# Kernel optimization log

Hardware: AMD Instinct MI355X
Metric: run time of the kernel (lower is better)

## Reference

```python
import jax, jax.numpy as jnp
import numpy as np

N_NODES = 50000
N_EDGES = 600000
N_GRAPHS = 512
HID = 128
LAT = 64
L = 4
BN_EPS = 1e-5


def _gelu(x):
    return jax.nn.gelu(x, approximate=False)


def _bn(x, g, b):
    m = jnp.mean(x, axis=0)
    v = jnp.var(x, axis=0)
    return (x - m) * jax.lax.rsqrt(v + BN_EPS) * g + b


def setup_inputs() -> dict:
    key = jax.random.key(0)
    ks = jax.random.split(key, 8)
    x = jax.random.normal(ks[0], (N_NODES, HID), dtype=jnp.float32)
    edge_index = jax.random.randint(ks[1], (2, N_EDGES), 0, N_NODES, dtype=jnp.int64 if jax.config.jax_enable_x64 else jnp.int32)
    batch = jnp.sort(jax.random.randint(ks[2], (N_NODES,), 0, N_GRAPHS))
    scale = 1.0 / np.sqrt(HID)
    return {
        "x": x,
        "edge_index": edge_index,
        "batch": batch,
        "input_bn_g": jnp.ones((HID,), jnp.float32),
        "input_bn_b": jnp.zeros((HID,), jnp.float32),
        "eps": jnp.zeros((L,), jnp.float32),
        "fc1_w": jax.random.normal(ks[3], (L, HID, HID), jnp.float32) * scale,
        "fc1_b": jnp.zeros((L, HID), jnp.float32),
        "bn1_g": jnp.ones((L, HID), jnp.float32),
        "bn1_b": jnp.zeros((L, HID), jnp.float32),
        "fc2_w": jax.random.normal(ks[4], (L, HID, HID), jnp.float32) * scale,
        "fc2_b": jnp.zeros((L, HID), jnp.float32),
        "bn_g": jnp.ones((L, HID), jnp.float32),
        "bn_b": jnp.zeros((L, HID), jnp.float32),
        "att_weight": jax.random.normal(ks[5], (L, HID), jnp.float32),
        "pool_weight": jnp.ones((3,), jnp.float32),
        "fcA_w": jax.random.normal(ks[6], (HID, HID), jnp.float32) * scale,
        "fcA_b": jnp.zeros((HID,), jnp.float32),
        "ln_g": jnp.ones((HID,), jnp.float32),
        "ln_b": jnp.zeros((HID,), jnp.float32),
        "fcB_w": jax.random.normal(ks[7], (HID, LAT), jnp.float32) * scale,
        "fcB_b": jnp.zeros((LAT,), jnp.float32),
    }


def reference(x, edge_index, batch, input_bn_g, input_bn_b, eps, fc1_w, fc1_b,
              bn1_g, bn1_b, fc2_w, fc2_b, bn_g, bn_b, att_weight, pool_weight,
              fcA_w, fcA_b, ln_g, ln_b, fcB_w, fcB_b):
    src, dst = edge_index[0], edge_index[1]
    x = _bn(x, input_bn_g, input_bn_b)  # input BatchNorm (batch stats)
    hidden_states = []
    for l in range(L):
        # GINConv: (1+eps)*x_i + sum_{j->i} x_j, then GatedResidualMLP
        agg = jax.ops.segment_sum(x[src], dst, num_segments=N_NODES)
        h = (1.0 + eps[l]) * x + agg
        h = _gelu(_bn(h @ fc1_w[l] + fc1_b[l], bn1_g[l], bn1_b[l]))
        h = h @ fc2_w[l] + fc2_b[l]
        h = _gelu(_bn(h, bn_g[l], bn_b[l]))
        hidden_states.append(h)
        x = h
    # JumpingKnowledge attention over layers
    x_all = jnp.stack(hidden_states, axis=0)               # [L, N, H]
    scores = jnp.mean(x_all * att_weight[:, None, :], -1)  # [L, N]
    alpha = jax.nn.softmax(scores, axis=0)
    x = jnp.sum(x_all * alpha[..., None], axis=0)          # [N, H]
    # fused add/mean/max pooling by graph id
    pw = jax.nn.softmax(pool_weight)
    sums = jax.ops.segment_sum(x, batch, num_segments=N_GRAPHS)
    cnt = jax.ops.segment_sum(jnp.ones((N_NODES, 1), x.dtype), batch, num_segments=N_GRAPHS)
    mean = sums / jnp.maximum(cnt, 1.0)
    mx = jax.ops.segment_max(x, batch, num_segments=N_GRAPHS)
    mx = jnp.where(cnt > 0, mx, 0.0)
    pooled = sums * pw[0] + mean * pw[1] + mx * pw[2]      # [G, H]
    out = pooled @ fcA_w + fcA_b
    mu = jnp.mean(out, -1, keepdims=True)
    var = jnp.var(out, -1, keepdims=True)
    out = (out - mu) * jax.lax.rsqrt(var + 1e-5) * ln_g + ln_b
    out = _gelu(out) + pooled
    return out @ fcB_w + fcB_b                              # [G, latent]
```

## Files before the change

### kernel.cpp

```cpp
#include <hip/hip_runtime.h>
#include <math.h>

#define N_NODES 50000
#define N_EDGES 600000
#define N_GRAPHS 512
#define HID 128
#define LAT 64
#define NL 4
#define SSTR 16
#define SSET 4096
#define N_TILES 3125
#define TLD 72

typedef __attribute__((ext_vector_type(8))) __bf16 bf16x8;
typedef __attribute__((ext_vector_type(4))) float f32x4;

union Chunk {
    bf16x8 v;
    uint4 u4;
    ushort us[8];
};

__device__ __forceinline__ float gelu_exact(float x) {
    return 0.5f * x * (1.0f + erff(x * 0.70710678118654752f));
}
__device__ __forceinline__ float gelu_fast(float x) {
    float ax = fabsf(x) * 0.70710678118654752f;
    float t = __builtin_amdgcn_rcpf(fmaf(0.3275911f, ax, 1.0f));
    float p = t * (0.254829592f +
              t * (-0.284496736f +
              t * (1.421413741f +
              t * (-1.453152027f + t * 1.061405429f))));
    float e = __expf(-ax * ax);
    float erfv = 1.0f - p * e;
    float erfs = copysignf(erfv, x);
    return 0.5f * x * (1.0f + erfs);
}
__device__ __forceinline__ float bf2f(ushort h) {
    return __uint_as_float(((unsigned int)h) << 16);
}
__device__ __forceinline__ ushort f2bf(float f) {
    unsigned int u = __float_as_uint(f);
    unsigned int r = (u + 0x7FFFu + ((u >> 16) & 1u)) >> 16;
    return (ushort)r;
}
__device__ __forceinline__ void atomicMaxF(float* addr, float v) {
    if (v >= 0.f) atomicMax((int*)addr, __float_as_int(v));
    else atomicMin((unsigned int*)addr, __float_as_uint(v));
}

__device__ __forceinline__ void sub_range(int p, int j, int& s0, int& s1) {
    int r0 = (p * N_NODES) >> 8;
    int r1 = ((p + 1) * N_NODES) >> 8;
    int len = r1 - r0;
    s0 = r0 + ((len * j) >> 3);
    s1 = r0 + ((len * (j + 1)) >> 3);
}

__global__ __launch_bounds__(256) void wt_build(const float* __restrict__ fc1w,
                                                const float* __restrict__ fc2w,
                                                ushort* __restrict__ Wt) {
    int i = blockIdx.x * 256 + threadIdx.x;
    if (i >= 8 * HID * HID) return;
    int g = i >> 14;
    int rem = i & 16383;
    int n = rem >> 7, k = rem & 127;
    const float* W = (g < 4) ? (fc1w + (long)g * HID * HID) : (fc2w + (long)(g - 4) * HID * HID);
    Wt[i] = f2bf(W[k * HID + n]);
}

__global__ __launch_bounds__(256) void col_stats(const float* __restrict__ X,
                                                 float* __restrict__ stats) {
    __shared__ float sh[2048];
    int t = threadIdx.x;
    int tx = t & 31, ty = t >> 5;
    float s[4] = {0, 0, 0, 0}, q[4] = {0, 0, 0, 0};
    const int nTiles = (N_NODES + 63) / 64;
    for (int tile = blockIdx.x; tile < nTiles; tile += gridDim.x) {
        int r0 = tile * 64;
#pragma unroll
        for (int i = 0; i < 8; ++i) {
            int r = r0 + ty + 8 * i;
            int rc = min(r, N_NODES - 1);
            float4 v = *(const float4*)(X + (long)rc * HID + 4 * tx);
            float w = (r < N_NODES) ? 1.f : 0.f;
            float x0 = v.x * w, x1 = v.y * w, x2 = v.z * w, x3 = v.w * w;
            s[0] += x0; s[1] += x1; s[2] += x2; s[3] += x3;
            q[0] += x0 * v.x; q[1] += x1 * v.y; q[2] += x2 * v.z; q[3] += x3 * v.w;
        }
    }
#pragma unroll
    for (int c = 0; c < 4; ++c) {
        sh[ty * HID + 4 * tx + c] = s[c];
        sh[1024 + ty * HID + 4 * tx + c] = q[c];
    }
    __syncthreads();
    if (ty == 0) {
#pragma unroll
        for (int c = 0; c < 4; ++c) {
            float a = 0, b = 0;
#pragma unroll
            for (int j = 0; j < 8; ++j) {
                a += sh[j * HID + 4 * tx + c];
                b += sh[1024 + j * HID + 4 * tx + c];
            }
            atomicAdd(stats + (4 * tx + c) * SSTR, a);
            atomicAdd(stats + (HID + 4 * tx + c) * SSTR, b);
        }
    }
}

__global__ __launch_bounds__(256) void bn_apply_f32(const float* __restrict__ X,
                                                    ushort* __restrict__ Y,
                                                    const float* __restrict__ stats,
                                                    const float* __restrict__ g,
                                                    const float* __restrict__ b) {
    __shared__ float scL[HID], sfL[HID];
    int t = threadIdx.x;
    if (t < HID) {
        const float invN = 1.0f / (float)N_NODES;
        float mean = stats[t * SSTR] * invN;
        float var = stats[(HID + t) * SSTR] * invN - mean * mean;
        float s = g[t] * rsqrtf(var + 1e-5f);
        scL[t] = s;
        sfL[t] = b[t] - mean * s;
    }
    __syncthreads();
    int c4 = (t & 31) * 4;
    float sc[4], sf[4];
#pragma unroll
    for (int j = 0; j < 4; ++j) { sc[j] = scL[c4 + j]; sf[j] = sfL[c4 + j]; }
    int s0, s1;
    sub_range(blockIdx.x & 255, blockIdx.x >> 8, s0, s1);
    int c0 = s0 * 32, c1 = s1 * 32;
    for (int i = c0 + t; i < c1; i += 256) {
        float4 v = ((const float4*)X)[i];
        ushort4 w;
        w.x = f2bf(v.x * sc[0] + sf[0]);
        w.y = f2bf(v.y * sc[1] + sf[1]);
        w.z = f2bf(v.z * sc[2] + sf[2]);
        w.w = f2bf(v.w * sc[3] + sf[3]);
        ((ushort4*)Y)[i] = w;
    }
}

__global__ __launch_bounds__(256) void bn_apply_bf(const ushort* __restrict__ X,
                                                   ushort* __restrict__ Y,
                                                   const float* __restrict__ stats,
                                                   const float* __restrict__ g,
                                                   const float* __restrict__ b) {
    __shared__ float scL[HID], sfL[HID];
    int t = threadIdx.x;
    if (t < HID) {
        const float invN = 1.0f / (float)N_NODES;
        float mean = stats[t * SSTR] * invN;
        float var = stats[(HID + t) * SSTR] * invN - mean * mean;
        float s = g[t] * rsqrtf(var + 1e-5f);
        scL[t] = s;
        sfL[t] = b[t] - mean * s;
    }
    __syncthreads();
    int c8 = (t & 15) * 8;
    float sc[8], sf[8];
#pragma unroll
    for (int j = 0; j < 8; ++j) { sc[j] = scL[c8 + j]; sf[j] = sfL[c8 + j]; }
    int s0, s1;
    sub_range(blockIdx.x & 255, blockIdx.x >> 8, s0, s1);
    int c0 = s0 * 16, c1 = s1 * 16;
    for (int i = c0 + t; i < c1; i += 256) {
        Chunk ch;
        ch.u4 = ((const uint4*)X)[i];
#pragma unroll
        for (int j = 0; j < 8; ++j) {
            float f = bf2f(ch.us[j]) * sc[j] + sf[j];
            ch.us[j] = f2bf(gelu_fast(f));
        }
        ((uint4*)Y)[i] = ch.u4;
    }
}

__global__ __launch_bounds__(256) void csr_count(const int* __restrict__ dst,
                                                 int* __restrict__ counts) {
    int e = blockIdx.x * blockDim.x + threadIdx.x;
    if (e >= N_EDGES) return;
    atomicAdd(counts + dst[e], 1);
}

__global__ __launch_bounds__(256) void scan_pass1(const int* __restrict__ counts,
                                                  int* __restrict__ offs,
                                                  int* __restrict__ bsum) {
    __shared__ int sh[256];
    int t = threadIdx.x;
    int i = blockIdx.x * 256 + t;
    int v = (i < N_NODES) ? counts[i] : 0;
    sh[t] = v;
    __syncthreads();
    for (int off = 1; off < 256; off <<= 1) {
        int a = (t >= off) ? sh[t - off] : 0;
        __syncthreads();
        sh[t] += a;
        __syncthreads();
    }
    if (i < N_NODES) offs[i] = sh[t] - v;
    if (t == 255) bsum[blockIdx.x] = sh[255];
}

__global__ __launch_bounds__(256) void scan_pass2(int* __restrict__ bsum, int nblk) {
    __shared__ int sh[256];
    int t = threadIdx.x;
    int v = (t < nblk) ? bsum[t] : 0;
    sh[t] = v;
    __syncthreads();
    for (int off = 1; off < 256; off <<= 1) {
        int a = (t >= off) ? sh[t - off] : 0;
        __syncthreads();
        sh[t] += a;
        __syncthreads();
    }
    if (t < nblk) bsum[t] = sh[t] - v;
}

__global__ __launch_bounds__(256) void scan_pass3(int* __restrict__ offs,
                                                  const int* __restrict__ bsum,
                                                  int* __restrict__ cursor) {
    int i = blockIdx.x * 256 + threadIdx.x;
    if (i >= N_NODES) return;
    int o = offs[i] + bsum[blockIdx.x];
    offs[i] = o;
    cursor[i] = o;
}

__global__ __launch_bounds__(256) void csr_fill(const int* __restrict__ src,
                                                const int* __restrict__ dst,
                                                int* __restrict__ cursor,
                                                int* __restrict__ csr) {
    int e = blockIdx.x * blockDim.x + threadIdx.x;
    if (e >= N_EDGES) return;
    int pos = atomicAdd(cursor + dst[e], 1);
    csr[pos] = src[e];
}

__global__ __launch_bounds__(256) void gin_gather_bf(const ushort* __restrict__ Xbf,
                                                     ushort* __restrict__ Hp,
                                                     const int* __restrict__ offs,
                                                     const int* __restrict__ counts,
                                                     const int* __restrict__ csr,
                                                     const float* __restrict__ eps, int l) {
    int t = threadIdx.x;
    int tx = t & 31;
    int grp = t >> 5;
    int s0, s1;
    sub_range(blockIdx.x & 255, blockIdx.x >> 8, s0, s1);
    float ev = 1.0f + eps[l];
    for (int node = s0 + grp; node < s1; node += 8) {
        ushort4 sv = *(const ushort4*)(Xbf + (long)node * HID + 4 * tx);
        float a0 = bf2f(sv.x) * ev, a1 = bf2f(sv.y) * ev;
        float a2 = bf2f(sv.z) * ev, a3 = bf2f(sv.w) * ev;
        int o = offs[node];
        int d = counts[node];
        int k = 0;
        for (; k + 8 <= d; k += 8) {
            int si[8];
#pragma unroll
            for (int j = 0; j < 8; ++j) si[j] = csr[o + k + j];
            ushort4 v[8];
#pragma unroll
            for (int j = 0; j < 8; ++j)
                v[j] = *(const ushort4*)(Xbf + (long)si[j] * HID + 4 * tx);
#pragma unroll
            for (int j = 0; j < 8; ++j) {
                a0 += bf2f(v[j].x); a1 += bf2f(v[j].y);
                a2 += bf2f(v[j].z); a3 += bf2f(v[j].w);
            }
        }
        for (; k + 4 <= d; k += 4) {
            int si[4];
#pragma unroll
            for (int j = 0; j < 4; ++j) si[j] = csr[o + k + j];
#pragma unroll
            for (int j = 0; j < 4; ++j) {
                ushort4 v = *(const ushort4*)(Xbf + (long)si[j] * HID + 4 * tx);
                a0 += bf2f(v.x); a1 += bf2f(v.y); a2 += bf2f(v.z); a3 += bf2f(v.w);
            }
        }
        for (; k < d; ++k) {
            int s = csr[o + k];
            ushort4 v = *(const ushort4*)(Xbf + (long)s * HID + 4 * tx);
            a0 += bf2f(v.x); a1 += bf2f(v.y); a2 += bf2f(v.z); a3 += bf2f(v.w);
        }
        ushort4 w;
        w.x = f2bf(a0); w.y = f2bf(a1); w.z = f2bf(a2); w.w = f2bf(a3);
        *(ushort4*)(Hp + (long)node * HID + 4 * tx) = w;
    }
}

__global__ __launch_bounds__(256, 1) void gemm_persist(
    const ushort* __restrict__ Abf, const ushort* __restrict__ Wt,
    const float* __restrict__ bias, ushort* __restrict__ Cbf,
    const float* __restrict__ statsIn, const float* __restrict__ gIn,
    const float* __restrict__ bIn, int applyIn, float* __restrict__ statsOut) {
    __shared__ float scL[HID], sfL[HID];
    __shared__ __align__(16) ushort T[4][16 * TLD];
    __shared__ float shs[8 * 64];
    int t = threadIdx.x;
    if (applyIn && t < HID) {
        const float invN = 1.0f / (float)N_NODES;
        float mean = statsIn[t * SSTR] * invN;
        float var = statsIn[(HID + t) * SSTR] * invN - mean * mean;
        float s = gIn[t] * rsqrtf(var + 1e-5f);
        scL[t] = s;
        sfL[t] = bIn[t] - mean * s;
    }
    __syncthreads();

    int w = t >> 6, lane = t & 63;
    int m = lane & 15, q = lane >> 4;
    int c2 = w & 1, r2 = w >> 1;
    ushort* Tw = T[w];

    const ushort* Wh = Wt + (long)(c2 * 64) * HID;
    bf16x8 Bfrag[4][4];
#pragma unroll
    for (int nt = 0; nt < 4; ++nt)
#pragma unroll
        for (int kc = 0; kc < 4; ++kc)
            Bfrag[nt][kc] = *(const bf16x8*)(Wh + (nt * 16 + m) * HID + kc * 32 + q * 8);

    float bias4[4];
#pragma unroll
    for (int nt = 0; nt < 4; ++nt) bias4[nt] = bias[c2 * 64 + nt * 16 + m];

    float s_col[4], q_col[4];
#pragma unroll
    for (int nt = 0; nt < 4; ++nt) { s_col[nt] = 0.f; q_col[nt] = 0.f; }

    int t0 = (blockIdx.x * N_TILES) >> 8;
    int t1 = ((blockIdx.x + 1) * N_TILES) >> 8;

    int tile = t0 + r2;
    Chunk Ac[4];
    if (tile < t1) {
        const ushort* arow = Abf + (long)(tile * 16 + m) * HID + q * 8;
#pragma unroll
        for (int kc = 0; kc < 4; ++kc) Ac[kc].u4 = *(const uint4*)(arow + kc * 32);
    }
    while (tile < t1) {
        int nxt = tile + 2;
        Chunk An[4];
        if (nxt < t1) {
            const ushort* arow = Abf + (long)(nxt * 16 + m) * HID + q * 8;
#pragma unroll
            for (int kc = 0; kc < 4; ++kc) An[kc].u4 = *(const uint4*)(arow + kc * 32);
        }
        if (applyIn) {
#pragma unroll
            for (int kc = 0; kc < 4; ++kc)
#pragma unroll
                for (int j = 0; j < 8; ++j) {
                    int k = kc * 32 + q * 8 + j;
                    float f = bf2f(Ac[kc].us[j]) * scL[k] + sfL[k];
                    Ac[kc].us[j] = f2bf(gelu_fast(f));
                }
        }
        f32x4 acc[4];
#pragma unroll
        for (int nt = 0; nt < 4; ++nt) acc[nt] = (f32x4){0.f, 0.f, 0.f, 0.f};
#pragma unroll
        for (int kc = 0; kc < 4; ++kc)
#pragma unroll
            for (int nt = 0; nt < 4; ++nt)
                acc[nt] = __builtin_amdgcn_mfma_f32_16x16x32_bf16(Ac[kc].v, Bfrag[nt][kc],
                                                                  acc[nt], 0, 0, 0);
#pragma unroll
        for (int nt = 0; nt < 4; ++nt) {
            int col = nt * 16 + m;
#pragma unroll
            for (int r = 0; r < 4; ++r) {
                float z = acc[nt][r] + bias4[nt];
                Tw[(q * 4 + r) * TLD + col] = f2bf(z);
                s_col[nt] += z;
                q_col[nt] += z * z;
            }
        }
        long cbase = (long)(tile * 16) * HID + c2 * 64;
#pragma unroll
        for (int i = 0; i < 2; ++i) {
            int slot = i * 64 + lane;
            int row = slot >> 3, off = slot & 7;
            uint4 vv = *(const uint4*)(Tw + row * TLD + off * 8);
            *(uint4*)(Cbf + cbase + (long)row * HID + off * 8) = vv;
        }
        tile = nxt;
#pragma unroll
        for (int kc = 0; kc < 4; ++kc) Ac[kc] = An[kc];
    }

#pragma unroll
    for (int nt = 0; nt < 4; ++nt) {
        s_col[nt] += __shfl_xor(s_col[nt], 16);
        s_col[nt] += __shfl_xor(s_col[nt], 32);
        q_col[nt] += __shfl_xor(q_col[nt], 16);
        q_col[nt] += __shfl_xor(q_col[nt], 32);
    }
    if (q == 0) {
#pragma unroll
        for (int nt = 0; nt < 4; ++nt) {
            shs[w * 64 + nt * 16 + m] = s_col[nt];
            shs[256 + w * 64 + nt * 16 + m] = q_col[nt];
        }
    }
    __syncthreads();
    if (t < HID) {
        int half = t >> 6, lc = t & 63;
        float a = shs[half * 64 + lc] + shs[(2 + half) * 64 + lc];
        float b = shs[256 + half * 64 + lc] + shs[256 + (2 + half) * 64 + lc];
        atomicAdd(statsOut + t * SSTR, a);
        atomicAdd(statsOut + (HID + t) * SSTR, b);
    }
}

__global__ __launch_bounds__(256) void pool_init(float* __restrict__ psum,
                                                 float* __restrict__ pmax,
                                                 int* __restrict__ gstart,
                                                 int* __restrict__ gend) {
    int i = blockIdx.x * 256 + threadIdx.x;
    if (i < N_GRAPHS) { gstart[i] = 0; gend[i] = 0; }
    if (i >= N_GRAPHS * HID) return;
    psum[i] = 0.f;
    pmax[i] = -INFINITY;
}

__global__ __launch_bounds__(256) void jk_pool(const ushort* __restrict__ H0,
                                               const ushort* __restrict__ H1,
                                               const ushort* __restrict__ H2,
                                               const ushort* __restrict__ H3,
                                               const float* __restrict__ att,
                                               const int* __restrict__ batch,
                                               float* __restrict__ psum,
                                               float* __restrict__ pmax) {
    int t = threadIdx.x;
    int lane = t & 63, w = t >> 6;
    long wid = (long)blockIdx.x * 4 + w;
    int a0 = (int)((wid * N_NODES) >> 13);
    int a1 = (int)(((wid + 1) * N_NODES) >> 13);
    const ushort* Hs[4] = {H0, H1, H2, H3};
    float2 av[4];
#pragma unroll
    for (int l = 0; l < 4; ++l) av[l] = *(const float2*)(att + l * HID + 2 * lane);

    int curg = -1;
    float sx = 0.f, sy = 0.f, mx = -INFINITY, my = -INFINITY;
    for (int node = a0; node < a1; ++node) {
        int g = batch[node];
        if (g != curg) {
            if (curg >= 0) {
                float* ps = psum + (long)curg * HID + 2 * lane;
                float* pm = pmax + (long)curg * HID + 2 * lane;
                atomicAdd(ps, sx);
                atomicAdd(ps + 1, sy);
                atomicMaxF(pm, mx);
                atomicMaxF(pm + 1, my);
            }
            curg = g;
            sx = 0.f; sy = 0.f; mx = -INFINITY; my = -INFINITY;
        }
        float hx[4], hy[4], scr[4];
#pragma unroll
        for (int l = 0; l < 4; ++l) {
            unsigned int u = *(const unsigned int*)(Hs[l] + (long)node * HID + 2 * lane);
            float vx = bf2f((ushort)(u & 0xFFFF));
            float vy = bf2f((ushort)(u >> 16));
            hx[l] = vx; hy[l] = vy;
            float p = vx * av[l].x + vy * av[l].y;
#pragma unroll
            for (int off = 32; off > 0; off >>= 1) p += __shfl_xor(p, off);
            scr[l] = p * (1.0f / HID);
        }
        float mm = fmaxf(fmaxf(scr[0], scr[1]), fmaxf(scr[2], scr[3]));
        float e[4], se = 0.f;
#pragma unroll
        for (int l = 0; l < 4; ++l) { e[l] = expf(scr[l] - mm); se += e[l]; }
        float inv = 1.0f / se;
        float ox = 0.f, oy = 0.f;
#pragma unroll
        for (int l = 0; l < 4; ++l) {
            float a = e[l] * inv;
            ox += a * hx[l];
            oy += a * hy[l];
        }
        sx += ox; sy += oy;
        mx = fmaxf(mx, ox); my = fmaxf(my, oy);
    }
    if (curg >= 0) {
        float* ps = psum + (long)curg * HID + 2 * lane;
        float* pm = pmax + (long)curg * HID + 2 * lane;
        atomicAdd(ps, sx);
        atomicAdd(ps + 1, sy);
        atomicMaxF(pm, mx);
        atomicMaxF(pm + 1, my);
    }
}

__global__ __launch_bounds__(128) void pool_finalize(const float* __restrict__ psum,
                                                     const float* __restrict__ pmax,
                                                     const int* __restrict__ gstart,
                                                     const int* __restrict__ gend,
                                                     const float* __restrict__ pw,
                                                     float* __restrict__ pooled) {
    int g = blockIdx.x, f = threadIdx.x;
    float w0 = pw[0], w1 = pw[1], w2 = pw[2];
    float m = fmaxf(w0, fmaxf(w1, w2));
    float e0 = expf(w0 - m), e1 = expf(w1 - m), e2 = expf(w2 - m);
    float inv = 1.0f / (e0 + e1 + e2);
    e0 *= inv; e1 *= inv; e2 *= inv;
    int cnt = gend[g] - gstart[g];
    float s = psum[g * HID + f];
    float mx = pmax[g * HID + f];
    float mean = cnt > 0 ? s / (float)cnt : 0.f;
    float mxv = cnt > 0 ? mx : 0.f;
    pooled[g * HID + f] = s * e0 + mean * e1 + mxv * e2;
}

__global__ void graph_ranges(const int* __restrict__ batch, int* __restrict__ gstart,
                             int* __restrict__ gend) {
    int n = blockIdx.x * blockDim.x + threadIdx.x;
    if (n >= N_NODES) return;
    int b = batch[n];
    if (n == 0 || batch[n - 1] != b) gstart[b] = n;
    if (n == N_NODES - 1 || batch[n + 1] != b) gend[b] = n + 1;
}

__global__ __launch_bounds__(128) void head_kernel(const float* __restrict__ pooled,
                                                   const float* __restrict__ fcAw,
                                                   const float* __restrict__ fcAb,
                                                   const float* __restrict__ lng,
                                                   const float* __restrict__ lnb,
                                                   const float* __restrict__ fcBw,
                                                   const float* __restrict__ fcBb,
                                                   float* __restrict__ out) {
    __shared__ float p[HID], q[HID], red[HID];
    int g = blockIdx.x, j = threadIdx.x;
    p[j] = pooled[g * HID + j];
    __syncthreads();
    float acc = fcAb[j];
    for (int k = 0; k < HID; ++k) acc += p[k] * fcAw[k * HID + j];
    red[j] = acc;
    __syncthreads();
    for (int off = 64; off > 0; off >>= 1) {
        if (j < off) red[j] += red[j + off];
        __syncthreads();
    }
    float mean = red[0] * (1.0f / HID);
    __syncthreads();
    float d = acc - mean;
    red[j] = d * d;
    __syncthreads();
    for (int off = 64; off > 0; off >>= 1) {
        if (j < off) red[j] += red[j + off];
        __syncthreads();
    }
    float var = red[0] * (1.0f / HID);
    float y = d * rsqrtf(var + 1e-5f) * lng[j] + lnb[j];
    q[j] = gelu_exact(y) + p[j];
    __syncthreads();
    if (j < LAT) {
        float o = fcBb[j];
        for (int k = 0; k < HID; ++k) o += q[k] * fcBw[k * LAT + j];
        out[g * LAT + j] = o;
    }
}

extern "C" void kernel_launch(void* const* d_in, const int* in_sizes, int n_in,
                              void* d_out, int out_size, void* d_ws, size_t ws_size,
                              hipStream_t stream) {
    const float* x = (const float*)d_in[0];
    const int* ei = (const int*)d_in[1];
    const int* src = ei;
    const int* dst = ei + N_EDGES;
    const int* batch = (const int*)d_in[2];
    const float* ibn_g = (const float*)d_in[3];
    const float* ibn_b = (const float*)d_in[4];
    const float* eps = (const float*)d_in[5];
    const float* fc1w = (const float*)d_in[6];
    const float* fc1b = (const float*)d_in[7];
    const float* bn1g = (const float*)d_in[8];
    const float* bn1b = (const float*)d_in[9];
    const float* fc2w = (const float*)d_in[10];
    const float* fc2b = (const float*)d_in[11];
    const float* bng = (const float*)d_in[12];
    const float* bnb = (const float*)d_in[13];
    const float* att = (const float*)d_in[14];
    const float* pw = (const float*)d_in[15];
    const float* fcAw = (const float*)d_in[16];
    const float* fcAb = (const float*)d_in[17];
    const float* lng = (const float*)d_in[18];
    const float* lnb = (const float*)d_in[19];
    const float* fcBw = (const float*)d_in[20];
    const float* fcBb = (const float*)d_in[21];
    float* out = (float*)d_out;

    const size_t NH = (size_t)N_NODES * HID;
    char* w8 = (char*)d_ws;
    ushort* x0bf = (ushort*)w8;     w8 += NH * 2;
    ushort* hprebf = (ushort*)w8;   w8 += NH * 2;
    ushort* z1bf = (ushort*)w8;     w8 += NH * 2;
    ushort* z2bf = (ushort*)w8;     w8 += NH * 2;
    ushort* Hlbf[NL];
    for (int l = 0; l < NL; ++l) { Hlbf[l] = (ushort*)w8; w8 += NH * 2; }
    float* statsAll = (float*)w8;   w8 += (size_t)9 * SSET * 4;
    float* psum = (float*)w8;       w8 += (size_t)N_GRAPHS * HID * 4;
    float* pmax = (float*)w8;       w8 += (size_t)N_GRAPHS * HID * 4;
    float* pooled = (float*)w8;     w8 += (size_t)N_GRAPHS * HID * 4;
    int* gstart = (int*)w8;         w8 += N_GRAPHS * 4;
    int* gend = (int*)w8;           w8 += N_GRAPHS * 4;
    int* counts = (int*)w8;         w8 += N_NODES * 4;
    int* offs = (int*)w8;           w8 += N_NODES * 4;
    int* cursor = (int*)w8;         w8 += N_NODES * 4;
    int* bsum = (int*)w8;           w8 += 256 * 4;
    int* csr = (int*)w8;            w8 += (size_t)N_EDGES * 4;
    ushort* WtBf = (ushort*)w8;     w8 += (size_t)8 * HID * HID * 2;

    const int nodeBlocks = (N_NODES + 255) / 256;
    const int edgeBlocks = (N_EDGES + 255) / 256;

    wt_build<<<512, 256, 0, stream>>>(fc1w, fc2w, WtBf);

    hipMemsetAsync(counts, 0, N_NODES * sizeof(int), stream);
    csr_count<<<edgeBlocks, 256, 0, stream>>>(dst, counts);
    scan_pass1<<<nodeBlocks, 256, 0, stream>>>(counts, offs, bsum);
    scan_pass2<<<1, 256, 0, stream>>>(bsum, nodeBlocks);
    scan_pass3<<<nodeBlocks, 256, 0, stream>>>(offs, bsum, cursor);
    csr_fill<<<edgeBlocks, 256, 0, stream>>>(src, dst, cursor, csr);
    pool_init<<<(N_GRAPHS * HID + 255) / 256, 256, 0, stream>>>(psum, pmax, gstart, gend);
    graph_ranges<<<nodeBlocks, 256, 0, stream>>>(batch, gstart, gend);

    hipMemsetAsync(statsAll, 0, (size_t)9 * SSET * sizeof(float), stream);

    col_stats<<<256, 256, 0, stream>>>(x, statsAll);
    bn_apply_f32<<<2048, 256, 0, stream>>>(x, x0bf, statsAll, ibn_g, ibn_b);

    const ushort* xin = x0bf;
    for (int l = 0; l < NL; ++l) {
        float* st1 = statsAll + (size_t)(1 + 2 * l) * SSET;
        float* st2 = statsAll + (size_t)(2 + 2 * l) * SSET;
        gin_gather_bf<<<2048, 256, 0, stream>>>(xin, hprebf, offs, counts, csr, eps, l);
        gemm_persist<<<256, 256, 0, stream>>>(hprebf, WtBf + (size_t)l * HID * HID,
                                              fc1b + l * HID, z1bf,
                                              nullptr, nullptr, nullptr, 0, st1);
        gemm_persist<<<256, 256, 0, stream>>>(z1bf, WtBf + (size_t)(4 + l) * HID * HID,
                                              fc2b + l * HID, z2bf,
                                              st1, bn1g + l * HID, bn1b + l * HID, 1, st2);
        bn_apply_bf<<<2048, 256, 0, stream>>>(z2bf, Hlbf[l], st2, bng + l * HID,
                                              bnb + l * HID);
        xin = Hlbf[l];
    }

    jk_pool<<<2048, 256, 0, stream>>>(Hlbf[0], Hlbf[1], Hlbf[2], Hlbf[3], att, batch,
                                      psum, pmax);
    pool_finalize<<<N_GRAPHS, 128, 0, stream>>>(psum, pmax, gstart, gend, pw, pooled);

    head_kernel<<<N_GRAPHS, 128, 0, stream>>>(pooled, fcAw, fcAb, lng, lnb, fcBw, fcBb, out);
}
```

Measured before the change: 525.9 us.

## Fuse per-layer MLP into persistent kernel with grid barriers; merge setup kernels

Replaces the two per-layer GEMM kernels and the BN-apply kernel with one persistent fused_mlp kernel. It keeps Z1/Z2 tiles in shared memory and uses a software grid barrier to wait for the batch-norm statistics between stages. Setup, counting, scan and pooling-finalize/head kernels are merged to cut launch count and memsets. This removes the global round trips of the z1/z2 intermediates and several launches. In exchange it relies on all 256 blocks being co-resident for the spin barrier, and its large LDS footprint limits occupancy.

After: 759.1 us. +44.3%, slower.

```diff
diff --git a/kernel.cpp b/kernel.cpp
--- a/kernel.cpp
+++ b/kernel.cpp
@@ -10,7 +10,8 @@
 #define SSTR 16
 #define SSET 4096
 #define N_TILES 3125
-#define TLD 72
+#define ZROWS 208
+#define ZLD 136
 
 typedef __attribute__((ext_vector_type(8))) __bf16 bf16x8;
 typedef __attribute__((ext_vector_type(4))) float f32x4;
@@ -57,65 +58,118 @@
     s1 = r0 + ((len * (j + 1)) >> 3);
 }
 
-__global__ __launch_bounds__(256) void wt_build(const float* __restrict__ fc1w,
-                                                const float* __restrict__ fc2w,
-                                                ushort* __restrict__ Wt) {
+__device__ __forceinline__ void grid_sync(int* bar) {
+    __syncthreads();
+    if (threadIdx.x == 0) {
+        int gen = __hip_atomic_load(bar + 1, __ATOMIC_RELAXED, __HIP_MEMORY_SCOPE_AGENT);
+        int prev = __hip_atomic_fetch_add(bar, 1, __ATOMIC_ACQ_REL, __HIP_MEMORY_SCOPE_AGENT);
+        if (prev == (int)gridDim.x - 1) {
+            __hip_atomic_store(bar, 0, __ATOMIC_RELAXED, __HIP_MEMORY_SCOPE_AGENT);
+            __hip_atomic_store(bar + 1, gen + 1, __ATOMIC_RELEASE, __HIP_MEMORY_SCOPE_AGENT);
+        } else {
+            while (__hip_atomic_load(bar + 1, __ATOMIC_RELAXED, __HIP_MEMORY_SCOPE_AGENT) == gen)
+                __builtin_amdgcn_s_sleep(8);
+        }
+    }
+    __syncthreads();
+    __threadfence();
+}
+
+__global__ __launch_bounds__(256) void setup(const float* __restrict__ fc1w,
+                                             const float* __restrict__ fc2w,
+                                             ushort* __restrict__ Wt,
+                                             int* __restrict__ counts,
+                                             float* __restrict__ statsAll,
+                                             float* __restrict__ psum,
+                                             float* __restrict__ pmax,
+                                             int* __restrict__ gstart,
+                                             int* __restrict__ gend,
+                                             int* __restrict__ bar) {
     int i = blockIdx.x * 256 + threadIdx.x;
-    if (i >= 8 * HID * HID) return;
-    int g = i >> 14;
-    int rem = i & 16383;
-    int n = rem >> 7, k = rem & 127;
-    const float* W = (g < 4) ? (fc1w + (long)g * HID * HID) : (fc2w + (long)(g - 4) * HID * HID);
-    Wt[i] = f2bf(W[k * HID + n]);
-}
-
-__global__ __launch_bounds__(256) void col_stats(const float* __restrict__ X,
-                                                 float* __restrict__ stats) {
+    {
+        int g = i >> 14;
+        int rem = i & 16383;
+        int n = rem >> 7, k = rem & 127;
+        const float* W = (g < 4) ? (fc1w + (long)g * HID * HID)
+                                 : (fc2w + (long)(g - 4) * HID * HID);
+        Wt[i] = f2bf(W[k * HID + n]);
+    }
+    if (i < N_NODES) counts[i] = 0;
+    if (i < 9 * SSET) statsAll[i] = 0.f;
+    if (i < N_GRAPHS * HID) { psum[i] = 0.f; pmax[i] = -INFINITY; }
+    if (i < N_GRAPHS) { gstart[i] = 0; gend[i] = 0; }
+    if (i < 8) bar[i] = 0;
+}
+
+__global__ __launch_bounds__(256) void stats_count(const float* __restrict__ X,
+                                                   float* __restrict__ stats,
+                                                   const int* __restrict__ dst,
+                                                   int* __restrict__ counts,
+                                                   const int* __restrict__ batch,
+                                                   int* __restrict__ gstart,
+                                                   int* __restrict__ gend) {
     __shared__ float sh[2048];
+    int bx = blockIdx.x;
     int t = threadIdx.x;
-    int tx = t & 31, ty = t >> 5;
-    float s[4] = {0, 0, 0, 0}, q[4] = {0, 0, 0, 0};
-    const int nTiles = (N_NODES + 63) / 64;
-    for (int tile = blockIdx.x; tile < nTiles; tile += gridDim.x) {
-        int r0 = tile * 64;
-#pragma unroll
-        for (int i = 0; i < 8; ++i) {
-            int r = r0 + ty + 8 * i;
-            int rc = min(r, N_NODES - 1);
-            float4 v = *(const float4*)(X + (long)rc * HID + 4 * tx);
-            float w = (r < N_NODES) ? 1.f : 0.f;
-            float x0 = v.x * w, x1 = v.y * w, x2 = v.z * w, x3 = v.w * w;
-            s[0] += x0; s[1] += x1; s[2] += x2; s[3] += x3;
-            q[0] += x0 * v.x; q[1] += x1 * v.y; q[2] += x2 * v.z; q[3] += x3 * v.w;
-        }
-    }
-#pragma unroll
-    for (int c = 0; c < 4; ++c) {
-        sh[ty * HID + 4 * tx + c] = s[c];
-        sh[1024 + ty * HID + 4 * tx + c] = q[c];
-    }
-    __syncthreads();
-    if (ty == 0) {
+    if (bx < 256) {
+        int tx = t & 31, ty = t >> 5;
+        float s[4] = {0, 0, 0, 0}, q[4] = {0, 0, 0, 0};
+        const int nTiles = (N_NODES + 63) / 64;
+        for (int tile = bx; tile < nTiles; tile += 256) {
+            int r0 = tile * 64;
+#pragma unroll
+            for (int i = 0; i < 8; ++i) {
+                int r = r0 + ty + 8 * i;
+                int rc = min(r, N_NODES - 1);
+                float4 v = *(const float4*)(X + (long)rc * HID + 4 * tx);
+                float w = (r < N_NODES) ? 1.f : 0.f;
+                float x0 = v.x * w, x1 = v.y * w, x2 = v.z * w, x3 = v.w * w;
+                s[0] += x0; s[1] += x1; s[2] += x2; s[3] += x3;
+                q[0] += x0 * v.x; q[1] += x1 * v.y; q[2] += x2 * v.z; q[3] += x3 * v.w;
+            }
+        }
 #pragma unroll
         for (int c = 0; c < 4; ++c) {
-            float a = 0, b = 0;
-#pragma unroll
-            for (int j = 0; j < 8; ++j) {
-                a += sh[j * HID + 4 * tx + c];
-                b += sh[1024 + j * HID + 4 * tx + c];
+            sh[ty * HID + 4 * tx + c] = s[c];
+            sh[1024 + ty * HID + 4 * tx + c] = q[c];
+        }
+        __syncthreads();
+        if (ty == 0) {
+#pragma unroll
+            for (int c = 0; c < 4; ++c) {
+                float a = 0, b = 0;
+#pragma unroll
+                for (int j = 0; j < 8; ++j) {
+                    a += sh[j * HID + 4 * tx + c];
+                    b += sh[1024 + j * HID + 4 * tx + c];
+                }
+                atomicAdd(stats + (4 * tx + c) * SSTR, a);
+                atomicAdd(stats + (HID + 4 * tx + c) * SSTR, b);
             }
-            atomicAdd(stats + (4 * tx + c) * SSTR, a);
-            atomicAdd(stats + (HID + 4 * tx + c) * SSTR, b);
-        }
-    }
-}
-
-__global__ __launch_bounds__(256) void bn_apply_f32(const float* __restrict__ X,
-                                                    ushort* __restrict__ Y,
-                                                    const float* __restrict__ stats,
-                                                    const float* __restrict__ g,
-                                                    const float* __restrict__ b) {
+        }
+    } else if (bx < 2600) {
+        int e = (bx - 256) * 256 + t;
+        if (e < N_EDGES) atomicAdd(counts + dst[e], 1);
+    } else {
+        int n = (bx - 2600) * 256 + t;
+        if (n < N_NODES) {
+            int b = batch[n];
+            if (n == 0 || batch[n - 1] != b) gstart[b] = n;
+            if (n == N_NODES - 1 || batch[n + 1] != b) gend[b] = n + 1;
+        }
+    }
+}
+
+__global__ __launch_bounds__(256) void bn_scan(const float* __restrict__ X,
+                                               ushort* __restrict__ Y,
+                                               const float* __restrict__ stats,
+                                               const float* __restrict__ g,
+                                               const float* __restrict__ b,
+                                               const int* __restrict__ counts,
+                                               int* __restrict__ offs,
+                                               int* __restrict__ bsum) {
     __shared__ float scL[HID], sfL[HID];
+    __shared__ int shI[256];
     int t = threadIdx.x;
     if (t < HID) {
         const float invN = 1.0f / (float)N_NODES;
@@ -142,92 +196,41 @@
         w.w = f2bf(v.w * sc[3] + sf[3]);
         ((ushort4*)Y)[i] = w;
     }
-}
-
-__global__ __launch_bounds__(256) void bn_apply_bf(const ushort* __restrict__ X,
-                                                   ushort* __restrict__ Y,
-                                                   const float* __restrict__ stats,
-                                                   const float* __restrict__ g,
-                                                   const float* __restrict__ b) {
-    __shared__ float scL[HID], sfL[HID];
-    int t = threadIdx.x;
-    if (t < HID) {
-        const float invN = 1.0f / (float)N_NODES;
-        float mean = stats[t * SSTR] * invN;
-        float var = stats[(HID + t) * SSTR] * invN - mean * mean;
-        float s = g[t] * rsqrtf(var + 1e-5f);
-        scL[t] = s;
-        sfL[t] = b[t] - mean * s;
-    }
-    __syncthreads();
-    int c8 = (t & 15) * 8;
-    float sc[8], sf[8];
-#pragma unroll
-    for (int j = 0; j < 8; ++j) { sc[j] = scL[c8 + j]; sf[j] = sfL[c8 + j]; }
-    int s0, s1;
-    sub_range(blockIdx.x & 255, blockIdx.x >> 8, s0, s1);
-    int c0 = s0 * 16, c1 = s1 * 16;
-    for (int i = c0 + t; i < c1; i += 256) {
-        Chunk ch;
-        ch.u4 = ((const uint4*)X)[i];
-#pragma unroll
-        for (int j = 0; j < 8; ++j) {
-            float f = bf2f(ch.us[j]) * sc[j] + sf[j];
-            ch.us[j] = f2bf(gelu_fast(f));
-        }
-        ((uint4*)Y)[i] = ch.u4;
-    }
-}
-
-__global__ __launch_bounds__(256) void csr_count(const int* __restrict__ dst,
-                                                 int* __restrict__ counts) {
-    int e = blockIdx.x * blockDim.x + threadIdx.x;
-    if (e >= N_EDGES) return;
-    atomicAdd(counts + dst[e], 1);
-}
-
-__global__ __launch_bounds__(256) void scan_pass1(const int* __restrict__ counts,
-                                                  int* __restrict__ offs,
-                                                  int* __restrict__ bsum) {
+    if (blockIdx.x < 196) {
+        int i = blockIdx.x * 256 + t;
+        int v = (i < N_NODES) ? counts[i] : 0;
+        shI[t] = v;
+        __syncthreads();
+        for (int off = 1; off < 256; off <<= 1) {
+            int a = (t >= off) ? shI[t - off] : 0;
+            __syncthreads();
+            shI[t] += a;
+            __syncthreads();
+        }
+        if (i < N_NODES) offs[i] = shI[t] - v;
+        if (t == 255) bsum[blockIdx.x] = shI[255];
+    }
+}
+
+__global__ __launch_bounds__(256) void scan23(int* __restrict__ offs,
+                                              const int* __restrict__ bsum,
+                                              int* __restrict__ cursor) {
     __shared__ int sh[256];
-    int t = threadIdx.x;
-    int i = blockIdx.x * 256 + t;
-    int v = (i < N_NODES) ? counts[i] : 0;
+    int t = threadIdx.x, bx = blockIdx.x;
+    int v = (t < bx) ? bsum[t] : 0;
     sh[t] = v;
     __syncthreads();
-    for (int off = 1; off < 256; off <<= 1) {
-        int a = (t >= off) ? sh[t - off] : 0;
+    for (int off = 128; off > 0; off >>= 1) {
+        if (t < off) sh[t] += sh[t + off];
         __syncthreads();
-        sh[t] += a;
-        __syncthreads();
-    }
-    if (i < N_NODES) offs[i] = sh[t] - v;
-    if (t == 255) bsum[blockIdx.x] = sh[255];
-}
-
-__global__ __launch_bounds__(256) void scan_pass2(int* __restrict__ bsum, int nblk) {
-    __shared__ int sh[256];
-    int t = threadIdx.x;
-    int v = (t < nblk) ? bsum[t] : 0;
-    sh[t] = v;
-    __syncthreads();
-    for (int off = 1; off < 256; off <<= 1) {
-        int a = (t >= off) ? sh[t - off] : 0;
-        __syncthreads();
-        sh[t] += a;
-        __syncthreads();
-    }
-    if (t < nblk) bsum[t] = sh[t] - v;
-}
-
-__global__ __launch_bounds__(256) void scan_pass3(int* __restrict__ offs,
-                                                  const int* __restrict__ bsum,
-                                                  int* __restrict__ cursor) {
-    int i = blockIdx.x * 256 + threadIdx.x;
-    if (i >= N_NODES) return;
-    int o = offs[i] + bsum[blockIdx.x];
-    offs[i] = o;
-    cursor[i] = o;
+    }
+    int pre = sh[0];
+    int i = bx * 256 + t;
+    if (i < N_NODES) {
+        int o = offs[i] + pre;
+        offs[i] = o;
+        cursor[i] = o;
+    }
 }
 
 __global__ __launch_bounds__(256) void csr_fill(const int* __restrict__ src,
@@ -294,73 +297,53 @@
     }
 }
 
-__global__ __launch_bounds__(256, 1) void gemm_persist(
-    const ushort* __restrict__ Abf, const ushort* __restrict__ Wt,
-    const float* __restrict__ bias, ushort* __restrict__ Cbf,
-    const float* __restrict__ statsIn, const float* __restrict__ gIn,
-    const float* __restrict__ bIn, int applyIn, float* __restrict__ statsOut) {
+__global__ __launch_bounds__(256, 1) void fused_mlp(
+    const ushort* __restrict__ Abf, const ushort* __restrict__ W1t,
+    const ushort* __restrict__ W2t, const float* __restrict__ b1v,
+    const float* __restrict__ b2v, const float* __restrict__ bn1g,
+    const float* __restrict__ bn1b, const float* __restrict__ bn2g,
+    const float* __restrict__ bn2b, float* __restrict__ st1,
+    float* __restrict__ st2, ushort* __restrict__ Hl, int* __restrict__ bar) {
+    __shared__ __align__(16) ushort Z1[ZROWS * ZLD];
+    __shared__ __align__(16) ushort Z2[ZROWS * ZLD];
+    __shared__ float shs[512];
     __shared__ float scL[HID], sfL[HID];
-    __shared__ __align__(16) ushort T[4][16 * TLD];
-    __shared__ float shs[8 * 64];
+
     int t = threadIdx.x;
-    if (applyIn && t < HID) {
-        const float invN = 1.0f / (float)N_NODES;
-        float mean = statsIn[t * SSTR] * invN;
-        float var = statsIn[(HID + t) * SSTR] * invN - mean * mean;
-        float s = gIn[t] * rsqrtf(var + 1e-5f);
-        scL[t] = s;
-        sfL[t] = bIn[t] - mean * s;
-    }
-    __syncthreads();
-
     int w = t >> 6, lane = t & 63;
     int m = lane & 15, q = lane >> 4;
     int c2 = w & 1, r2 = w >> 1;
-    ushort* Tw = T[w];
-
-    const ushort* Wh = Wt + (long)(c2 * 64) * HID;
-    bf16x8 Bfrag[4][4];
-#pragma unroll
-    for (int nt = 0; nt < 4; ++nt)
-#pragma unroll
-        for (int kc = 0; kc < 4; ++kc)
-            Bfrag[nt][kc] = *(const bf16x8*)(Wh + (nt * 16 + m) * HID + kc * 32 + q * 8);
-
-    float bias4[4];
-#pragma unroll
-    for (int nt = 0; nt < 4; ++nt) bias4[nt] = bias[c2 * 64 + nt * 16 + m];
-
-    float s_col[4], q_col[4];
-#pragma unroll
-    for (int nt = 0; nt < 4; ++nt) { s_col[nt] = 0.f; q_col[nt] = 0.f; }
-
     int t0 = (blockIdx.x * N_TILES) >> 8;
     int t1 = ((blockIdx.x + 1) * N_TILES) >> 8;
 
+    bf16x8 Bf[4][4];
+    {
+        const ushort* Wh = W1t + (long)(c2 * 64) * HID;
+#pragma unroll
+        for (int nt = 0; nt < 4; ++nt)
+#pragma unroll
+            for (int kc = 0; kc < 4; ++kc)
+                Bf[nt][kc] = *(const bf16x8*)(Wh + (nt * 16 + m) * HID + kc * 32 + q * 8);
+    }
+    float bias4[4];
+#pragma unroll
+    for (int nt = 0; nt < 4; ++nt) bias4[nt] = b1v[c2 * 64 + nt * 16 + m];
+
+    float s_c[4] = {0, 0, 0, 0}, q_c[4] = {0, 0, 0, 0};
     int tile = t0 + r2;
     Chunk Ac[4];
     if (tile < t1) {
-        const ushort* arow = Abf + (long)(tile * 16 + m) * HID + q * 8;
-#pragma unroll
-        for (int kc = 0; kc < 4; ++kc) Ac[kc].u4 = *(const uint4*)(arow + kc * 32);
+        const ushort* ar = Abf + (long)(tile * 16 + m) * HID + q * 8;
+#pragma unroll
+        for (int kc = 0; kc < 4; ++kc) Ac[kc].u4 = *(const uint4*)(ar + kc * 32);
     }
     while (tile < t1) {
         int nxt = tile + 2;
         Chunk An[4];
         if (nxt < t1) {
-            const ushort* arow = Abf + (long)(nxt * 16 + m) * HID + q * 8;
-#pragma unroll
-            for (int kc = 0; kc < 4; ++kc) An[kc].u4 = *(const uint4*)(arow + kc * 32);
-        }
-        if (applyIn) {
-#pragma unroll
-            for (int kc = 0; kc < 4; ++kc)
-#pragma unroll
-                for (int j = 0; j < 8; ++j) {
-                    int k = kc * 32 + q * 8 + j;
-                    float f = bf2f(Ac[kc].us[j]) * scL[k] + sfL[k];
-                    Ac[kc].us[j] = f2bf(gelu_fast(f));
-                }
+            const ushort* ar = Abf + (long)(nxt * 16 + m) * HID + q * 8;
+#pragma unroll
+            for (int kc = 0; kc < 4; ++kc) An[kc].u4 = *(const uint4*)(ar + kc * 32);
         }
         f32x4 acc[4];
 #pragma unroll
@@ -369,44 +352,36 @@
         for (int kc = 0; kc < 4; ++kc)
 #pragma unroll
             for (int nt = 0; nt < 4; ++nt)
-                acc[nt] = __builtin_amdgcn_mfma_f32_16x16x32_bf16(Ac[kc].v, Bfrag[nt][kc],
+                acc[nt] = __builtin_amdgcn_mfma_f32_16x16x32_bf16(Ac[kc].v, Bf[nt][kc],
                                                                   acc[nt], 0, 0, 0);
+        int lrow = (tile - t0) * 16;
 #pragma unroll
         for (int nt = 0; nt < 4; ++nt) {
-            int col = nt * 16 + m;
+            int col = c2 * 64 + nt * 16 + m;
 #pragma unroll
             for (int r = 0; r < 4; ++r) {
                 float z = acc[nt][r] + bias4[nt];
-                Tw[(q * 4 + r) * TLD + col] = f2bf(z);
-                s_col[nt] += z;
-                q_col[nt] += z * z;
+                Z1[(lrow + q * 4 + r) * ZLD + col] = f2bf(z);
+                s_c[nt] += z;
+                q_c[nt] += z * z;
             }
         }
-        long cbase = (long)(tile * 16) * HID + c2 * 64;
-#pragma unroll
-        for (int i = 0; i < 2; ++i) {
-            int slot = i * 64 + lane;
-            int row = slot >> 3, off = slot & 7;
-            uint4 vv = *(const uint4*)(Tw + row * TLD + off * 8);
-            *(uint4*)(Cbf + cbase + (long)row * HID + off * 8) = vv;
-        }
         tile = nxt;
 #pragma unroll
         for (int kc = 0; kc < 4; ++kc) Ac[kc] = An[kc];
     }
-
 #pragma unroll
     for (int nt = 0; nt < 4; ++nt) {
-        s_col[nt] += __shfl_xor(s_col[nt], 16);
-        s_col[nt] += __shfl_xor(s_col[nt], 32);
-        q_col[nt] += __shfl_xor(q_col[nt], 16);
-        q_col[nt] += __shfl_xor(q_col[nt], 32);
+        s_c[nt] += __shfl_xor(s_c[nt], 16);
+        s_c[nt] += __shfl_xor(s_c[nt], 32);
+        q_c[nt] += __shfl_xor(q_c[nt], 16);
+        q_c[nt] += __shfl_xor(q_c[nt], 32);
     }
     if (q == 0) {
 #pragma unroll
         for (int nt = 0; nt < 4; ++nt) {
-            shs[w * 64 + nt * 16 + m] = s_col[nt];
-            shs[256 + w * 64 + nt * 16 + m] = q_col[nt];
+            shs[w * 64 + nt * 16 + m] = s_c[nt];
+            shs[256 + w * 64 + nt * 16 + m] = q_c[nt];
         }
     }
     __syncthreads();
@@ -414,20 +389,116 @@
         int half = t >> 6, lc = t & 63;
         float a = shs[half * 64 + lc] + shs[(2 + half) * 64 + lc];
         float b = shs[256 + half * 64 + lc] + shs[256 + (2 + half) * 64 + lc];
-        atomicAdd(statsOut + t * SSTR, a);
-        atomicAdd(statsOut + (HID + t) * SSTR, b);
-    }
-}
-
-__global__ __launch_bounds__(256) void pool_init(float* __restrict__ psum,
-                                                 float* __restrict__ pmax,
-                                                 int* __restrict__ gstart,
-                                                 int* __restrict__ gend) {
-    int i = blockIdx.x * 256 + threadIdx.x;
-    if (i < N_GRAPHS) { gstart[i] = 0; gend[i] = 0; }
-    if (i >= N_GRAPHS * HID) return;
-    psum[i] = 0.f;
-    pmax[i] = -INFINITY;
+        atomicAdd(st1 + t * SSTR, a);
+        atomicAdd(st1 + (HID + t) * SSTR, b);
+    }
+    grid_sync(bar);
+
+    if (t < HID) {
+        const float invN = 1.0f / (float)N_NODES;
+        float mean = st1[t * SSTR] * invN;
+        float var = st1[(HID + t) * SSTR] * invN - mean * mean;
+        float s = bn1g[t] * rsqrtf(var + 1e-5f);
+        scL[t] = s;
+        sfL[t] = bn1b[t] - mean * s;
+    }
+    __syncthreads();
+
+    {
+        const ushort* Wh = W2t + (long)(c2 * 64) * HID;
+#pragma unroll
+        for (int nt = 0; nt < 4; ++nt)
+#pragma unroll
+            for (int kc = 0; kc < 4; ++kc)
+                Bf[nt][kc] = *(const bf16x8*)(Wh + (nt * 16 + m) * HID + kc * 32 + q * 8);
+    }
+#pragma unroll
+    for (int nt = 0; nt < 4; ++nt) bias4[nt] = b2v[c2 * 64 + nt * 16 + m];
+#pragma unroll
+    for (int nt = 0; nt < 4; ++nt) { s_c[nt] = 0.f; q_c[nt] = 0.f; }
+
+    for (int tl = t0 + r2; tl < t1; tl += 2) {
+        int lrow = (tl - t0) * 16;
+        Chunk Ax[4];
+#pragma unroll
+        for (int kc = 0; kc < 4; ++kc)
+            Ax[kc].u4 = *(const uint4*)(Z1 + (lrow + m) * ZLD + kc * 32 + q * 8);
+#pragma unroll
+        for (int kc = 0; kc < 4; ++kc)
+#pragma unroll
+            for (int j = 0; j < 8; ++j) {
+                int k = kc * 32 + q * 8 + j;
+                float f = bf2f(Ax[kc].us[j]) * scL[k] + sfL[k];
+                Ax[kc].us[j] = f2bf(gelu_fast(f));
+            }
+        f32x4 acc[4];
+#pragma unroll
+        for (int nt = 0; nt < 4; ++nt) acc[nt] = (f32x4){0.f, 0.f, 0.f, 0.f};
+#pragma unroll
+        for (int kc = 0; kc < 4; ++kc)
+#pragma unroll
+            for (int nt = 0; nt < 4; ++nt)
+                acc[nt] = __builtin_amdgcn_mfma_f32_16x16x32_bf16(Ax[kc].v, Bf[nt][kc],
+                                                                  acc[nt], 0, 0, 0);
+#pragma unroll
+        for (int nt = 0; nt < 4; ++nt) {
+            int col = c2 * 64 + nt * 16 + m;
+#pragma unroll
+            for (int r = 0; r < 4; ++r) {
+                float z = acc[nt][r] + bias4[nt];
+                Z2[(lrow + q * 4 + r) * ZLD + col] = f2bf(z);
+                s_c[nt] += z;
+                q_c[nt] += z * z;
+            }
+        }
+    }
+#pragma unroll
+    for (int nt = 0; nt < 4; ++nt) {
+        s_c[nt] += __shfl_xor(s_c[nt], 16);
+        s_c[nt] += __shfl_xor(s_c[nt], 32);
+        q_c[nt] += __shfl_xor(q_c[nt], 16);
+        q_c[nt] += __shfl_xor(q_c[nt], 32);
+    }
+    if (q == 0) {
+#pragma unroll
+        for (int nt = 0; nt < 4; ++nt) {
+            shs[w * 64 + nt * 16 + m] = s_c[nt];
+            shs[256 + w * 64 + nt * 16 + m] = q_c[nt];
+        }
+    }
+    __syncthreads();
+    if (t < HID) {
+        int half = t >> 6, lc = t & 63;
+        float a = shs[half * 64 + lc] + shs[(2 + half) * 64 + lc];
+        float b = shs[256 + half * 64 + lc] + shs[256 + (2 + half) * 64 + lc];
+        atomicAdd(st2 + t * SSTR, a);
+        atomicAdd(st2 + (HID + t) * SSTR, b);
+    }
+    grid_sync(bar);
+
+    if (t < HID) {
+        const float invN = 1.0f / (float)N_NODES;
+        float mean = st2[t * SSTR] * invN;
+        float var = st2[(HID + t) * SSTR] * invN - mean * mean;
+        float s = bn2g[t] * rsqrtf(var + 1e-5f);
+        scL[t] = s;
+        sfL[t] = bn2b[t] - mean * s;
+    }
+    __syncthreads();
+
+    int nch = (t1 - t0) * 16 * 16;
+    for (int i = t; i < nch; i += 256) {
+        int row = i >> 4, off = i & 15;
+        Chunk ch;
+        ch.u4 = *(const uint4*)(Z2 + row * ZLD + off * 8);
+#pragma unroll
+        for (int j = 0; j < 8; ++j) {
+            int cc = off * 8 + j;
+            float f = bf2f(ch.us[j]) * scL[cc] + sfL[cc];
+            ch.us[j] = f2bf(gelu_fast(f));
+        }
+        *(uint4*)(Hl + (long)(t0 * 16 + row) * HID + off * 8) = ch.u4;
+    }
 }
 
 __global__ __launch_bounds__(256) void jk_pool(const ushort* __restrict__ H0,
@@ -501,46 +572,32 @@
     }
 }
 
-__global__ __launch_bounds__(128) void pool_finalize(const float* __restrict__ psum,
+__global__ __launch_bounds__(128) void finalize_head(const float* __restrict__ psum,
                                                      const float* __restrict__ pmax,
                                                      const int* __restrict__ gstart,
                                                      const int* __restrict__ gend,
                                                      const float* __restrict__ pw,
-                                                     float* __restrict__ pooled) {
-    int g = blockIdx.x, f = threadIdx.x;
+                                                     const float* __restrict__ fcAw,
+                                                     const float* __restrict__ fcAb,
+                                                     const float* __restrict__ lng,
+                                                     const float* __restrict__ lnb,
+                                                     const float* __restrict__ fcBw,
+                                                     const float* __restrict__ fcBb,
+                                                     float* __restrict__ out) {
+    __shared__ float p[HID], qv[HID], red[HID];
+    int g = blockIdx.x, j = threadIdx.x;
     float w0 = pw[0], w1 = pw[1], w2 = pw[2];
-    float m = fmaxf(w0, fmaxf(w1, w2));
-    float e0 = expf(w0 - m), e1 = expf(w1 - m), e2 = expf(w2 - m);
+    float mw = fmaxf(w0, fmaxf(w1, w2));
+    float e0 = expf(w0 - mw), e1 = expf(w1 - mw), e2 = expf(w2 - mw);
     float inv = 1.0f / (e0 + e1 + e2);
     e0 *= inv; e1 *= inv; e2 *= inv;
     int cnt = gend[g] - gstart[g];
-    float s = psum[g * HID + f];
-    float mx = pmax[g * HID + f];
-    float mean = cnt > 0 ? s / (float)cnt : 0.f;
+    float s = psum[g * HID + j];
+    float mx = pmax[g * HID + j];
+    float mean0 = cnt > 0 ? s / (float)cnt : 0.f;
     float mxv = cnt > 0 ? mx : 0.f;
-    pooled[g * HID + f] = s * e0 + mean * e1 + mxv * e2;
-}
-
-__global__ void graph_ranges(const int* __restrict__ batch, int* __restrict__ gstart,
-                             int* __restrict__ gend) {
-    int n = blockIdx.x * blockDim.x + threadIdx.x;
-    if (n >= N_NODES) return;
-    int b = batch[n];
-    if (n == 0 || batch[n - 1] != b) gstart[b] = n;
-    if (n == N_NODES - 1 || batch[n + 1] != b) gend[b] = n + 1;
-}
-
-__global__ __launch_bounds__(128) void head_kernel(const float* __restrict__ pooled,
-                                                   const float* __restrict__ fcAw,
-                                                   const float* __restrict__ fcAb,
-                                                   const float* __restrict__ lng,
-                                                   const float* __restrict__ lnb,
-                                                   const float* __restrict__ fcBw,
-                                                   const float* __restrict__ fcBb,
-                                                   float* __restrict__ out) {
-    __shared__ float p[HID], q[HID], red[HID];
-    int g = blockIdx.x, j = threadIdx.x;
-    p[j] = pooled[g * HID + j];
+    float pool = s * e0 + mean0 * e1 + mxv * e2;
+    p[j] = pool;
     __syncthreads();
     float acc = fcAb[j];
     for (int k = 0; k < HID; ++k) acc += p[k] * fcAw[k * HID + j];
@@ -561,11 +618,11 @@
     }
     float var = red[0] * (1.0f / HID);
     float y = d * rsqrtf(var + 1e-5f) * lng[j] + lnb[j];
-    q[j] = gelu_exact(y) + p[j];
+    qv[j] = gelu_exact(y) + pool;
     __syncthreads();
     if (j < LAT) {
         float o = fcBb[j];
-        for (int k = 0; k < HID; ++k) o += q[k] * fcBw[k * LAT + j];
+        for (int k = 0; k < HID; ++k) o += qv[k] * fcBw[k * LAT + j];
         out[g * LAT + j] = o;
     }
 }
@@ -603,14 +660,11 @@
     char* w8 = (char*)d_ws;
     ushort* x0bf = (ushort*)w8;     w8 += NH * 2;
     ushort* hprebf = (ushort*)w8;   w8 += NH * 2;
-    ushort* z1bf = (ushort*)w8;     w8 += NH * 2;
-    ushort* z2bf = (ushort*)w8;     w8 += NH * 2;
     ushort* Hlbf[NL];
     for (int l = 0; l < NL; ++l) { Hlbf[l] = (ushort*)w8; w8 += NH * 2; }
     float* statsAll = (float*)w8;   w8 += (size_t)9 * SSET * 4;
     float* psum = (float*)w8;       w8 += (size_t)N_GRAPHS * HID * 4;
     float* pmax = (float*)w8;       w8 += (size_t)N_GRAPHS * HID * 4;
-    float* pooled = (float*)w8;     w8 += (size_t)N_GRAPHS * HID * 4;
     int* gstart = (int*)w8;         w8 += N_GRAPHS * 4;
     int* gend = (int*)w8;           w8 += N_GRAPHS * 4;
     int* counts = (int*)w8;         w8 += N_NODES * 4;
@@ -619,45 +673,35 @@
     int* bsum = (int*)w8;           w8 += 256 * 4;
     int* csr = (int*)w8;            w8 += (size_t)N_EDGES * 4;
     ushort* WtBf = (ushort*)w8;     w8 += (size_t)8 * HID * HID * 2;
-
-    const int nodeBlocks = (N_NODES + 255) / 256;
+    int* bar = (int*)w8;            w8 += 64 * 4;
+
     const int edgeBlocks = (N_EDGES + 255) / 256;
 
-    wt_build<<<512, 256, 0, stream>>>(fc1w, fc2w, WtBf);
-
-    hipMemsetAsync(counts, 0, N_NODES * sizeof(int), stream);
-    csr_count<<<edgeBlocks, 256, 0, stream>>>(dst, counts);
-    scan_pass1<<<nodeBlocks, 256, 0, stream>>>(counts, offs, bsum);
-    scan_pass2<<<1, 256, 0, stream>>>(bsum, nodeBlocks);
-    scan_pass3<<<nodeBlocks, 256, 0, stream>>>(offs, bsum, cursor);
+    setup<<<512, 256, 0, stream>>>(fc1w, fc2w, WtBf, counts, statsAll, psum, pmax,
+                                   gstart, gend, bar);
+    stats_count<<<256 + edgeBlocks + 196, 256, 0, stream>>>(x, statsAll, dst, counts,
+                                                            batch, gstart, gend);
+    bn_scan<<<2048, 256, 0, stream>>>(x, x0bf, statsAll, ibn_g, ibn_b, counts, offs,
+                                      bsum);
+    scan23<<<196, 256, 0, stream>>>(offs, bsum, cursor);
     csr_fill<<<edgeBlocks, 256, 0, stream>>>(src, dst, cursor, csr);
-    pool_init<<<(N_GRAPHS * HID + 255) / 256, 256, 0, stream>>>(psum, pmax, gstart, gend);
-    graph_ranges<<<nodeBlocks, 256, 0, stream>>>(batch, gstart, gend);
-
-    hipMemsetAsync(statsAll, 0, (size_t)9 * SSET * sizeof(float), stream);
-
-    col_stats<<<256, 256, 0, stream>>>(x, statsAll);
-    bn_apply_f32<<<2048, 256, 0, stream>>>(x, x0bf, statsAll, ibn_g, ibn_b);
 
     const ushort* xin = x0bf;
     for (int l = 0; l < NL; ++l) {
         float* st1 = statsAll + (size_t)(1 + 2 * l) * SSET;
         float* st2 = statsAll + (size_t)(2 + 2 * l) * SSET;
         gin_gather_bf<<<2048, 256, 0, stream>>>(xin, hprebf, offs, counts, csr, eps, l);
-        gemm_persist<<<256, 256, 0, stream>>>(hprebf, WtBf + (size_t)l * HID * HID,
-                                              fc1b + l * HID, z1bf,
-                                              nullptr, nullptr, nullptr, 0, st1);
-        gemm_persist<<<256, 256, 0, stream>>>(z1bf, WtBf + (size_t)(4 + l) * HID * HID,
-                                              fc2b + l * HID, z2bf,
-                                              st1, bn1g + l * HID, bn1b + l * HID, 1, st2);
-        bn_apply_bf<<<2048, 256, 0, stream>>>(z2bf, Hlbf[l], st2, bng + l * HID,
-                                              bnb + l * HID);
+        fused_mlp<<<256, 256, 0, stream>>>(hprebf, WtBf + (size_t)l * HID * HID,
+                                           WtBf + (size_t)(4 + l) * HID * HID,
+                                           fc1b + l * HID, fc2b + l * HID,
+                                           bn1g + l * HID, bn1b + l * HID,
+                                           bng + l * HID, bnb + l * HID,
+                                           st1, st2, Hlbf[l], bar);
         xin = Hlbf[l];
     }
 
     jk_pool<<<2048, 256, 0, stream>>>(Hlbf[0], Hlbf[1], Hlbf[2], Hlbf[3], att, batch,
                                       psum, pmax);
-    pool_finalize<<<N_GRAPHS, 128, 0, stream>>>(psum, pmax, gstart, gend, pw, pooled);
-
-    head_kernel<<<N_GRAPHS, 128, 0, stream>>>(pooled, fcAw, fcAb, lng, lnb, fcBw, fcBb, out);
-}
+    finalize_head<<<N_GRAPHS, 128, 0, stream>>>(psum, pmax, gstart, gend, pw, fcAw,
+                                                fcAb, lng, lnb, fcBw, fcBb, out);
+}
```
